# Optimization experiments

Hardware: AMD Instinct MI355X
Metric: run time of the kernel (lower is better)

The kernel has to match this reference:

```python
import jax, jax.numpy as jnp
import numpy as np

N_NODES = 50000
N_EDGES = 800000
IN_CH = 128
HEADS = 2
OUT_CH = 64
NEG_SLOPE = 0.2


def setup_inputs() -> dict:
    key = jax.random.key(0)
    ks = jax.random.split(key, 8)
    x = jax.random.normal(ks[0], (N_NODES, IN_CH), dtype=jnp.float32)
    # edges with no self-loops (module strips them anyway before re-adding)
    src = jax.random.randint(ks[1], (N_EDGES,), 0, N_NODES)
    off = jax.random.randint(ks[2], (N_EDGES,), 1, N_NODES)
    dst = (src + off) % N_NODES
    edge_index = jnp.stack([src, dst]).astype(jnp.int64)
    sc = 1.0 / np.sqrt(IN_CH)
    Wl = jax.random.normal(ks[3], (IN_CH, HEADS * OUT_CH), dtype=jnp.float32) * sc
    att_l = jax.random.normal(ks[4], (1, HEADS, OUT_CH), dtype=jnp.float32) * 0.1
    att_r = jax.random.normal(ks[5], (1, HEADS, OUT_CH), dtype=jnp.float32) * 0.1
    Wout = jax.random.normal(ks[6], (HEADS * OUT_CH, OUT_CH), dtype=jnp.float32) * (1.0 / np.sqrt(HEADS * OUT_CH))
    bias = jnp.zeros((OUT_CH,), dtype=jnp.float32)
    return {"x": x, "edge_index": edge_index, "Wl": Wl, "att_l": att_l,
            "att_r": att_r, "Wout": Wout, "bias": bias}


def reference(x, edge_index, Wl, att_l, att_r, Wout, bias):
    N = x.shape[0]
    H, C = att_l.shape[1], att_l.shape[2]
    # input edges have no self-loops; module removes then re-adds them
    loops = jnp.arange(N, dtype=edge_index.dtype)
    src = jnp.concatenate([edge_index[0], loops])  # j (source / neighbor)
    dst = jnp.concatenate([edge_index[1], loops])  # i (target / aggregation index)
    # shared lin_l == lin_r projection -> [N, H, C]
    xh = (x @ Wl).reshape(N, H, C)
    alpha_l = jnp.sum(xh * att_l, axis=-1)  # [N, H]
    alpha_r = jnp.sum(xh * att_r, axis=-1)  # [N, H]
    # per-edge attention logits: alpha_j + alpha_i, then LeakyReLU
    e = jax.nn.leaky_relu(alpha_l[src] + alpha_r[dst], negative_slope=NEG_SLOPE)  # [E, H]
    # segment softmax over destination nodes (numerically stable)
    emax = jax.ops.segment_max(e, dst, num_segments=N)
    emax = jnp.where(jnp.isfinite(emax), emax, 0.0)
    ex = jnp.exp(e - emax[dst])
    denom = jax.ops.segment_sum(ex, dst, num_segments=N)
    alpha = ex / (denom[dst] + 1e-16)  # matches PyG softmax eps
    # weighted scatter-add aggregation of source features
    msg = xh[src] * alpha[:, :, None]                # [E, H, C]
    out = jax.ops.segment_sum(msg, dst, num_segments=N)  # [N, H, C]
    # concat heads -> output projection + bias (concat=True, bias=True path)
    out = out.reshape(N, H * C) @ Wout + bias
    return out
```

## Files before the change

kernel.cpp:

```cpp
#include <hip/hip_runtime.h>

#define NEG_SLOPE 0.2f

static __device__ __forceinline__ unsigned short f2bf(float f) {
    unsigned u = __float_as_uint(f);
    unsigned r = (u + 0x7fffu + ((u >> 16) & 1u)) >> 16;
    return (unsigned short)r;
}
static __device__ __forceinline__ float bflo(unsigned z) {
    return __uint_as_float((z & 0xffffu) << 16);
}
static __device__ __forceinline__ float bfhi(unsigned z) {
    return __uint_as_float(z & 0xffff0000u);
}

__global__ __launch_bounds__(256) void prep_kernel(
    const float* __restrict__ Wl, const float* __restrict__ Wout,
    const float* __restrict__ attL, const float* __restrict__ attR,
    float* __restrict__ Wc, float* __restrict__ avec)
{
    int idx = blockIdx.x * 256 + threadIdx.x;
    if (idx < 128 * 128) {
        int k = idx >> 7, c = idx & 127;
        int h = c >> 6, cc = c & 63;
        const float* wl = Wl + k * 128 + h * 64;
        const float* wo = Wout + (h * 64) * 64 + cc;
        float s = 0.f;
#pragma unroll 8
        for (int m = 0; m < 64; ++m) s += wl[m] * wo[m * 64];
        Wc[k * 128 + c] = s;
    } else if (idx < 128 * 128 + 512) {
        int r = idx - 128 * 128;
        int k = r >> 2, t = r & 3;
        int h = t & 1;
        const float* av = ((t < 2) ? attL : attR) + h * 64;
        const float* wl = Wl + k * 128 + h * 64;
        float s = 0.f;
#pragma unroll 8
        for (int m = 0; m < 64; ++m) s += wl[m] * av[m];
        avec[k * 4 + t] = s;
    }
}

__global__ __launch_bounds__(256, 4) void zproj_kernel(
    const float* __restrict__ x, const float* __restrict__ Wc,
    const float* __restrict__ avec, int N,
    unsigned short* __restrict__ Z, float* __restrict__ AL, float* __restrict__ AR)
{
    __shared__ float xs[64 * 136];
    __shared__ float avs[128 * 4];
    const int tid = threadIdx.x;
    const int row0 = blockIdx.x * 64;

    const float4* x4 = (const float4*)x;
#pragma unroll
    for (int it = 0; it < 8; ++it) {
        int f4 = it * 256 + tid;
        int r = f4 >> 5, kq = f4 & 31;
        int rsrc = row0 + r; if (rsrc >= N) rsrc = N - 1;
        float4 v = x4[(size_t)rsrc * 32 + kq];
        *(float4*)&xs[r * 136 + kq * 4] = v;
    }
    if (tid < 128) *(float4*)&avs[tid * 4] = *(const float4*)&avec[tid * 4];
    __syncthreads();

    const int cg = tid & 31;
    const int rg = tid >> 5;
    const int c0 = cg * 4, r0 = rg * 8;
    float acc[8][4] = {};
    const float* wp = Wc + c0;
    for (int kc = 0; kc < 32; ++kc) {
        int k = kc * 4;
        float4 w0 = *(const float4*)&wp[(k + 0) * 128];
        float4 w1 = *(const float4*)&wp[(k + 1) * 128];
        float4 w2 = *(const float4*)&wp[(k + 2) * 128];
        float4 w3 = *(const float4*)&wp[(k + 3) * 128];
#pragma unroll
        for (int i = 0; i < 8; ++i) {
            float4 xv = *(const float4*)&xs[(r0 + i) * 136 + k];
            acc[i][0] += xv.x * w0.x + xv.y * w1.x + xv.z * w2.x + xv.w * w3.x;
            acc[i][1] += xv.x * w0.y + xv.y * w1.y + xv.z * w2.y + xv.w * w3.y;
            acc[i][2] += xv.x * w0.z + xv.y * w1.z + xv.z * w2.z + xv.w * w3.z;
            acc[i][3] += xv.x * w0.w + xv.y * w1.w + xv.z * w2.w + xv.w * w3.w;
        }
    }
#pragma unroll
    for (int i = 0; i < 8; ++i) {
        int row = row0 + r0 + i;
        if (row < N) {
            ushort4 zz;
            zz.x = f2bf(acc[i][0]); zz.y = f2bf(acc[i][1]);
            zz.z = f2bf(acc[i][2]); zz.w = f2bf(acc[i][3]);
            *(ushort4*)(Z + (size_t)row * 128 + c0) = zz;
        }
    }
    {
        int row = tid >> 2, t = tid & 3;
        const float* xr = &xs[row * 136];
        float s = 0.f;
#pragma unroll 8
        for (int k = 0; k < 128; k += 4) {
            float4 xv = *(const float4*)&xr[k];
            s += xv.x * avs[(k + 0) * 4 + t] + xv.y * avs[(k + 1) * 4 + t]
               + xv.z * avs[(k + 2) * 4 + t] + xv.w * avs[(k + 3) * 4 + t];
        }
        int grow = row0 + row;
        if (grow < N) {
            if (t < 2) AL[grow * 2 + t] = s;
            else       AR[grow * 2 + (t - 2)] = s;
        }
    }
}

__global__ void count_kernel(const int* __restrict__ ei, int E, int Etot,
                             int* __restrict__ cnt)
{
    int e = blockIdx.x * 256 + threadIdx.x;
    if (e >= Etot) return;
    int dst = (e < E) ? ei[E + e] : (e - E);
    atomicAdd(&cnt[dst], 1);
}

__global__ __launch_bounds__(256) void scan1(const int* __restrict__ cnt, int N,
                                             int* __restrict__ off, int* __restrict__ chs)
{
    __shared__ int s[256];
    int t = threadIdx.x, i = blockIdx.x * 256 + t;
    int v = (i < N) ? cnt[i] : 0;
    s[t] = v; __syncthreads();
#pragma unroll
    for (int o = 1; o < 256; o <<= 1) {
        int add = (t >= o) ? s[t - o] : 0;
        __syncthreads();
        s[t] += add;
        __syncthreads();
    }
    if (i < N) off[i] = s[t] - v;
    if (t == 255) chs[blockIdx.x] = s[255];
}

__global__ __launch_bounds__(256) void scan2(int* __restrict__ chs, int nb)
{
    __shared__ int s[256];
    int t = threadIdx.x;
    int v = (t < nb) ? chs[t] : 0;
    s[t] = v; __syncthreads();
#pragma unroll
    for (int o = 1; o < 256; o <<= 1) {
        int add = (t >= o) ? s[t - o] : 0;
        __syncthreads();
        s[t] += add;
        __syncthreads();
    }
    if (t < nb) chs[t] = s[t] - v;
}

__global__ void scan3(int* __restrict__ off, const int* __restrict__ chs, int N)
{
    int i = blockIdx.x * 256 + threadIdx.x;
    if (i < N) off[i] += chs[i >> 8];
}

__global__ void fill_kernel(const int* __restrict__ ei, int E, int Etot,
                            const float* __restrict__ AL, const float* __restrict__ AR,
                            int* __restrict__ off, float4* __restrict__ edg)
{
    int e = blockIdx.x * 256 + threadIdx.x;
    if (e >= Etot) return;
    int src, dst;
    if (e < E) { src = ei[e]; dst = ei[E + e]; }
    else       { src = e - E; dst = e - E; }
    float2 al = *(const float2*)&AL[src * 2];
    float2 ar = *(const float2*)&AR[dst * 2];
    float e0 = al.x + ar.x, e1 = al.y + ar.y;
    e0 = (e0 < 0.f) ? NEG_SLOPE * e0 : e0;
    e1 = (e1 < 0.f) ? NEG_SLOPE * e1 : e1;
    int pos = atomicAdd(&off[dst], 1);
    float4 rec;
    rec.x = __int_as_float(src);
    rec.y = __expf(e0);
    rec.z = __expf(e1);
    rec.w = 0.f;
    edg[pos] = rec;
}

__global__ __launch_bounds__(256) void agg_kernel(
    const int* __restrict__ off, const int* __restrict__ cnt,
    const float4* __restrict__ edg, const unsigned short* __restrict__ Z,
    const float* __restrict__ bias, float* __restrict__ out, int N)
{
    int wid = threadIdx.x >> 6, lane = threadIdx.x & 63;
    int node = blockIdx.x * 4 + wid;
    if (node >= N) return;
    int end = off[node];
    int start = end - cnt[node];
    int h2 = lane >> 5;
    int l5 = lane & 31;
    int head = l5 >> 4;
    float a0 = 0.f, a1 = 0.f, a2 = 0.f, a3 = 0.f, ws = 0.f;
    for (int e = start; e < end; e += 2) {
        float4 r0 = edg[e];
        float4 r1 = (e + 1 < end) ? edg[e + 1] : make_float4(r0.x, 0.f, 0.f, 0.f);
        float4 rc = h2 ? r1 : r0;
        int j = __float_as_int(rc.x);
        float w = head ? rc.z : rc.y;
        uint2 zz = *(const uint2*)(Z + (size_t)j * 128 + l5 * 4);
        a0 += w * bflo(zz.x); a1 += w * bfhi(zz.x);
        a2 += w * bflo(zz.y); a3 += w * bfhi(zz.y);
        ws += w;
    }
    a0 += __shfl_xor(a0, 32); a1 += __shfl_xor(a1, 32);
    a2 += __shfl_xor(a2, 32); a3 += __shfl_xor(a3, 32);
    ws += __shfl_xor(ws, 32);
    float inv = 1.f / (ws + 1e-16f);
    a0 *= inv; a1 *= inv; a2 *= inv; a3 *= inv;
    a0 += __shfl_xor(a0, 16); a1 += __shfl_xor(a1, 16);
    a2 += __shfl_xor(a2, 16); a3 += __shfl_xor(a3, 16);
    if (lane < 16) {
        float4 bv = *(const float4*)&bias[lane * 4];
        float4 o = make_float4(a0 + bv.x, a1 + bv.y, a2 + bv.z, a3 + bv.w);
        *(float4*)&out[(size_t)node * 64 + lane * 4] = o;
    }
}

extern "C" void kernel_launch(void* const* d_in, const int* in_sizes, int n_in,
                              void* d_out, int out_size, void* d_ws, size_t ws_size,
                              hipStream_t stream)
{
    const float* x    = (const float*)d_in[0];
    const int*   ei   = (const int*)d_in[1];
    const float* Wl   = (const float*)d_in[2];
    const float* attL = (const float*)d_in[3];
    const float* attR = (const float*)d_in[4];
    const float* Wout = (const float*)d_in[5];
    const float* bias = (const float*)d_in[6];
    float* out = (float*)d_out;

    const int N = in_sizes[0] / 128;
    const int E = in_sizes[1] / 2;
    const int Etot = E + N;

    char* ws = (char*)d_ws;
    size_t o = 0;
    auto alloc = [&](size_t bytes) {
        void* p = ws + o; o += (bytes + 255) & ~(size_t)255; return p;
    };
    float*          Wc   = (float*)alloc(128 * 128 * 4);
    float*          AV   = (float*)alloc(128 * 4 * 4);
    unsigned short* Z    = (unsigned short*)alloc((size_t)N * 128 * 2);
    float*          AL   = (float*)alloc((size_t)N * 2 * 4);
    float*          AR   = (float*)alloc((size_t)N * 2 * 4);
    int*            CNT  = (int*)alloc((size_t)N * 4);
    int*            OFF  = (int*)alloc((size_t)N * 4);
    int*            CHS  = (int*)alloc(256 * 4);
    float4*         EDG  = (float4*)alloc((size_t)Etot * 16);

    hipMemsetAsync(CNT, 0, (size_t)N * 4, stream);

    prep_kernel<<<66, 256, 0, stream>>>(Wl, Wout, attL, attR, Wc, AV);
    zproj_kernel<<<(N + 63) / 64, 256, 0, stream>>>(x, Wc, AV, N, Z, AL, AR);

    int eb = (Etot + 255) / 256;
    count_kernel<<<eb, 256, 0, stream>>>(ei, E, Etot, CNT);
    int nb = (N + 255) / 256;
    scan1<<<nb, 256, 0, stream>>>(CNT, N, OFF, CHS);
    scan2<<<1, 256, 0, stream>>>(CHS, nb);
    scan3<<<nb, 256, 0, stream>>>(OFF, CHS, N);
    fill_kernel<<<eb, 256, 0, stream>>>(ei, E, Etot, AL, AR, OFF, EDG);

    agg_kernel<<<(N + 3) / 4, 256, 0, stream>>>(OFF, CNT, EDG, Z, bias, out, N);
}
```

Before: 272.6 us.

## Fuse prep/count and zproj/scan kernels, shrink edge records, widen aggregation

Merges the weight-prep and degree-count launches into one grid, and the projection and first-level scan into another. The third scan pass is dropped by adding the chunk base on the fly in fill and agg. Edge records shrink from 16 to 8 bytes by packing the two exp weights as fp16. The aggregation now processes four edges per step with 16-byte Z loads and prefetches the next record. This cuts launch count and edge-buffer traffic, at the cost of fp16 precision on the attention weights and an extra chs lookup per access.

Measured after the change: 231.0 us. -15.3%, faster.

```diff
diff --git a/kernel.cpp b/kernel.cpp
--- a/kernel.cpp
+++ b/kernel.cpp
@@ -1,4 +1,5 @@
 #include <hip/hip_runtime.h>
+#include <hip/hip_fp16.h>
 
 #define NEG_SLOPE 0.2f
 
@@ -14,44 +15,74 @@
     return __uint_as_float(z & 0xffff0000u);
 }
 
-__global__ __launch_bounds__(256) void prep_kernel(
+#define PREP_B 66
+
+__global__ __launch_bounds__(256) void prep_count_kernel(
     const float* __restrict__ Wl, const float* __restrict__ Wout,
     const float* __restrict__ attL, const float* __restrict__ attR,
-    float* __restrict__ Wc, float* __restrict__ avec)
-{
-    int idx = blockIdx.x * 256 + threadIdx.x;
-    if (idx < 128 * 128) {
-        int k = idx >> 7, c = idx & 127;
-        int h = c >> 6, cc = c & 63;
-        const float* wl = Wl + k * 128 + h * 64;
-        const float* wo = Wout + (h * 64) * 64 + cc;
-        float s = 0.f;
+    float* __restrict__ Wc, float* __restrict__ avec,
+    const int* __restrict__ ei, int E, int Etot, int* __restrict__ cnt)
+{
+    int bid = blockIdx.x;
+    if (bid < PREP_B) {
+        int idx = bid * 256 + threadIdx.x;
+        if (idx < 128 * 128) {
+            int k = idx >> 7, c = idx & 127;
+            int h = c >> 6, cc = c & 63;
+            const float* wl = Wl + k * 128 + h * 64;
+            const float* wo = Wout + (h * 64) * 64 + cc;
+            float s = 0.f;
 #pragma unroll 8
-        for (int m = 0; m < 64; ++m) s += wl[m] * wo[m * 64];
-        Wc[k * 128 + c] = s;
-    } else if (idx < 128 * 128 + 512) {
-        int r = idx - 128 * 128;
-        int k = r >> 2, t = r & 3;
-        int h = t & 1;
-        const float* av = ((t < 2) ? attL : attR) + h * 64;
-        const float* wl = Wl + k * 128 + h * 64;
-        float s = 0.f;
+            for (int m = 0; m < 64; ++m) s += wl[m] * wo[m * 64];
+            Wc[k * 128 + c] = s;
+        } else if (idx < 128 * 128 + 512) {
+            int r = idx - 128 * 128;
+            int k = r >> 2, t = r & 3;
+            int h = t & 1;
+            const float* av = ((t < 2) ? attL : attR) + h * 64;
+            const float* wl = Wl + k * 128 + h * 64;
+            float s = 0.f;
 #pragma unroll 8
-        for (int m = 0; m < 64; ++m) s += wl[m] * av[m];
-        avec[k * 4 + t] = s;
-    }
-}
-
-__global__ __launch_bounds__(256, 4) void zproj_kernel(
+            for (int m = 0; m < 64; ++m) s += wl[m] * av[m];
+            avec[k * 4 + t] = s;
+        }
+    } else {
+        int e = (bid - PREP_B) * 256 + threadIdx.x;
+        if (e >= Etot) return;
+        int dst = (e < E) ? ei[E + e] : (e - E);
+        atomicAdd(&cnt[dst], 1);
+    }
+}
+
+__global__ __launch_bounds__(256, 4) void zproj_scan_kernel(
     const float* __restrict__ x, const float* __restrict__ Wc,
-    const float* __restrict__ avec, int N,
-    unsigned short* __restrict__ Z, float* __restrict__ AL, float* __restrict__ AR)
+    const float* __restrict__ avec, int N, int ZB,
+    unsigned short* __restrict__ Z, float* __restrict__ AL, float* __restrict__ AR,
+    const int* __restrict__ cnt, int* __restrict__ off, int* __restrict__ chs)
 {
     __shared__ float xs[64 * 136];
     __shared__ float avs[128 * 4];
     const int tid = threadIdx.x;
+
+    if ((int)blockIdx.x >= ZB) {
+        int blk = blockIdx.x - ZB;
+        int* s = (int*)xs;
+        int i = blk * 256 + tid;
+        int v = (i < N) ? cnt[i] : 0;
+        s[tid] = v; __syncthreads();
+#pragma unroll
+        for (int o = 1; o < 256; o <<= 1) {
+            int add = (tid >= o) ? s[tid - o] : 0;
+            __syncthreads();
+            s[tid] += add;
+            __syncthreads();
+        }
+        if (i < N) off[i] = s[tid] - v;
+        if (tid == 255) chs[blk] = s[255];
+        return;
+    }
+
     const int row0 = blockIdx.x * 64;
-
     const float4* x4 = (const float4*)x;
 #pragma unroll
     for (int it = 0; it < 8; ++it) {
@@ -112,21 +143,11 @@
     }
 }
 
-__global__ void count_kernel(const int* __restrict__ ei, int E, int Etot,
-                             int* __restrict__ cnt)
-{
-    int e = blockIdx.x * 256 + threadIdx.x;
-    if (e >= Etot) return;
-    int dst = (e < E) ? ei[E + e] : (e - E);
-    atomicAdd(&cnt[dst], 1);
-}
-
-__global__ __launch_bounds__(256) void scan1(const int* __restrict__ cnt, int N,
-                                             int* __restrict__ off, int* __restrict__ chs)
+__global__ __launch_bounds__(256) void scan2(int* __restrict__ chs, int nb)
 {
     __shared__ int s[256];
-    int t = threadIdx.x, i = blockIdx.x * 256 + t;
-    int v = (i < N) ? cnt[i] : 0;
+    int t = threadIdx.x;
+    int v = (t < nb) ? chs[t] : 0;
     s[t] = v; __syncthreads();
 #pragma unroll
     for (int o = 1; o < 256; o <<= 1) {
@@ -135,35 +156,13 @@
         s[t] += add;
         __syncthreads();
     }
-    if (i < N) off[i] = s[t] - v;
-    if (t == 255) chs[blockIdx.x] = s[255];
-}
-
-__global__ __launch_bounds__(256) void scan2(int* __restrict__ chs, int nb)
-{
-    __shared__ int s[256];
-    int t = threadIdx.x;
-    int v = (t < nb) ? chs[t] : 0;
-    s[t] = v; __syncthreads();
-#pragma unroll
-    for (int o = 1; o < 256; o <<= 1) {
-        int add = (t >= o) ? s[t - o] : 0;
-        __syncthreads();
-        s[t] += add;
-        __syncthreads();
-    }
     if (t < nb) chs[t] = s[t] - v;
-}
-
-__global__ void scan3(int* __restrict__ off, const int* __restrict__ chs, int N)
-{
-    int i = blockIdx.x * 256 + threadIdx.x;
-    if (i < N) off[i] += chs[i >> 8];
 }
 
 __global__ void fill_kernel(const int* __restrict__ ei, int E, int Etot,
                             const float* __restrict__ AL, const float* __restrict__ AR,
-                            int* __restrict__ off, float4* __restrict__ edg)
+                            int* __restrict__ off, const int* __restrict__ chs,
+                            uint2* __restrict__ edg)
 {
     int e = blockIdx.x * 256 + threadIdx.x;
     if (e >= Etot) return;
@@ -175,51 +174,67 @@
     float e0 = al.x + ar.x, e1 = al.y + ar.y;
     e0 = (e0 < 0.f) ? NEG_SLOPE * e0 : e0;
     e1 = (e1 < 0.f) ? NEG_SLOPE * e1 : e1;
-    int pos = atomicAdd(&off[dst], 1);
-    float4 rec;
-    rec.x = __int_as_float(src);
-    rec.y = __expf(e0);
-    rec.z = __expf(e1);
-    rec.w = 0.f;
+    int pos = atomicAdd(&off[dst], 1) + chs[dst >> 8];
+    __half2 hh = __floats2half2_rn(__expf(e0), __expf(e1));
+    uint2 rec;
+    rec.x = (unsigned)src;
+    rec.y = *(unsigned*)&hh;
     edg[pos] = rec;
 }
 
 __global__ __launch_bounds__(256) void agg_kernel(
-    const int* __restrict__ off, const int* __restrict__ cnt,
-    const float4* __restrict__ edg, const unsigned short* __restrict__ Z,
-    const float* __restrict__ bias, float* __restrict__ out, int N)
+    const int* __restrict__ off, const int* __restrict__ chs,
+    const int* __restrict__ cnt, const uint2* __restrict__ edg,
+    const unsigned short* __restrict__ Z, const float* __restrict__ bias,
+    float* __restrict__ out, int N)
 {
     int wid = threadIdx.x >> 6, lane = threadIdx.x & 63;
     int node = blockIdx.x * 4 + wid;
     if (node >= N) return;
-    int end = off[node];
+    int base = chs[node >> 8];
+    int end  = base + off[node];
     int start = end - cnt[node];
-    int h2 = lane >> 5;
-    int l5 = lane & 31;
-    int head = l5 >> 4;
-    float a0 = 0.f, a1 = 0.f, a2 = 0.f, a3 = 0.f, ws = 0.f;
-    for (int e = start; e < end; e += 2) {
-        float4 r0 = edg[e];
-        float4 r1 = (e + 1 < end) ? edg[e + 1] : make_float4(r0.x, 0.f, 0.f, 0.f);
-        float4 rc = h2 ? r1 : r0;
-        int j = __float_as_int(rc.x);
-        float w = head ? rc.z : rc.y;
-        uint2 zz = *(const uint2*)(Z + (size_t)j * 128 + l5 * 4);
-        a0 += w * bflo(zz.x); a1 += w * bfhi(zz.x);
-        a2 += w * bflo(zz.y); a3 += w * bfhi(zz.y);
+    int g  = lane >> 4;
+    int l4 = lane & 15;
+    int h  = l4 >> 3;
+    float a[8] = {};
+    float ws = 0.f;
+    uint2 rec = make_uint2(0u, 0u);
+    if (start + g < end) rec = edg[start + g];
+    for (int e = start; e < end; e += 4) {
+        uint2 nrec = make_uint2(0u, 0u);
+        int ne = e + 4 + g;
+        if (ne < end) nrec = edg[ne];
+        int j = (int)rec.x;
+        unsigned hv = h ? (rec.y >> 16) : (rec.y & 0xffffu);
+        float w = __half2float(__ushort_as_half((unsigned short)hv));
+        uint4 zz = *(const uint4*)(Z + (size_t)j * 128 + l4 * 8);
+        a[0] += w * bflo(zz.x); a[1] += w * bfhi(zz.x);
+        a[2] += w * bflo(zz.y); a[3] += w * bfhi(zz.y);
+        a[4] += w * bflo(zz.z); a[5] += w * bfhi(zz.z);
+        a[6] += w * bflo(zz.w); a[7] += w * bfhi(zz.w);
         ws += w;
-    }
-    a0 += __shfl_xor(a0, 32); a1 += __shfl_xor(a1, 32);
-    a2 += __shfl_xor(a2, 32); a3 += __shfl_xor(a3, 32);
+        rec = nrec;
+    }
+#pragma unroll
+    for (int i = 0; i < 8; ++i) {
+        a[i] += __shfl_xor(a[i], 16);
+        a[i] += __shfl_xor(a[i], 32);
+    }
+    ws += __shfl_xor(ws, 16);
     ws += __shfl_xor(ws, 32);
     float inv = 1.f / (ws + 1e-16f);
-    a0 *= inv; a1 *= inv; a2 *= inv; a3 *= inv;
-    a0 += __shfl_xor(a0, 16); a1 += __shfl_xor(a1, 16);
-    a2 += __shfl_xor(a2, 16); a3 += __shfl_xor(a3, 16);
-    if (lane < 16) {
-        float4 bv = *(const float4*)&bias[lane * 4];
-        float4 o = make_float4(a0 + bv.x, a1 + bv.y, a2 + bv.z, a3 + bv.w);
-        *(float4*)&out[(size_t)node * 64 + lane * 4] = o;
+#pragma unroll
+    for (int i = 0; i < 8; ++i) a[i] *= inv;
+#pragma unroll
+    for (int i = 0; i < 8; ++i) a[i] += __shfl_xor(a[i], 8);
+    if (lane < 8) {
+        float4 b0 = *(const float4*)&bias[lane * 8];
+        float4 b1 = *(const float4*)&bias[lane * 8 + 4];
+        float4 o0 = make_float4(a[0] + b0.x, a[1] + b0.y, a[2] + b0.z, a[3] + b0.w);
+        float4 o1 = make_float4(a[4] + b1.x, a[5] + b1.y, a[6] + b1.z, a[7] + b1.w);
+        *(float4*)&out[(size_t)node * 64 + lane * 8] = o0;
+        *(float4*)&out[(size_t)node * 64 + lane * 8 + 4] = o1;
     }
 }
 
@@ -253,20 +268,19 @@
     int*            CNT  = (int*)alloc((size_t)N * 4);
     int*            OFF  = (int*)alloc((size_t)N * 4);
     int*            CHS  = (int*)alloc(256 * 4);
-    float4*         EDG  = (float4*)alloc((size_t)Etot * 16);
+    uint2*          EDG  = (uint2*)alloc((size_t)Etot * 8);
 
     hipMemsetAsync(CNT, 0, (size_t)N * 4, stream);
 
-    prep_kernel<<<66, 256, 0, stream>>>(Wl, Wout, attL, attR, Wc, AV);
-    zproj_kernel<<<(N + 63) / 64, 256, 0, stream>>>(x, Wc, AV, N, Z, AL, AR);
-
     int eb = (Etot + 255) / 256;
-    count_kernel<<<eb, 256, 0, stream>>>(ei, E, Etot, CNT);
     int nb = (N + 255) / 256;
-    scan1<<<nb, 256, 0, stream>>>(CNT, N, OFF, CHS);
+    int ZB = (N + 63) / 64;
+
+    prep_count_kernel<<<PREP_B + eb, 256, 0, stream>>>(Wl, Wout, attL, attR,
+                                                       Wc, AV, ei, E, Etot, CNT);
+    zproj_scan_kernel<<<ZB + nb, 256, 0, stream>>>(x, Wc, AV, N, ZB,
+                                                   Z, AL, AR, CNT, OFF, CHS);
     scan2<<<1, 256, 0, stream>>>(CHS, nb);
-    scan3<<<nb, 256, 0, stream>>>(OFF, CHS, N);
-    fill_kernel<<<eb, 256, 0, stream>>>(ei, E, Etot, AL, AR, OFF, EDG);
-
-    agg_kernel<<<(N + 3) / 4, 256, 0, stream>>>(OFF, CNT, EDG, Z, bias, out, N);
-}
+    fill_kernel<<<eb, 256, 0, stream>>>(ei, E, Etot, AL, AR, OFF, CHS, EDG);
+    agg_kernel<<<(N + 3) / 4, 256, 0, stream>>>(OFF, CHS, CNT, EDG, Z, bias, out, N);
+}
```
